# Kernel tuning notes

Measured on AMD Instinct MI355X. Metric: run time of the kernel, lower is better.

## Reference

```python
import jax, jax.numpy as jnp
import numpy as np

B, T, C = 2, 2048, 1024
NH = 16
HD = C // NH

def setup_inputs() -> dict:
    key = jax.random.key(0)
    k1, k2, k3 = jax.random.split(key, 3)
    x = jax.random.normal(k1, (B, T, C), dtype=jnp.float32)
    w_attn = jax.random.normal(k2, (C, 3 * C), dtype=jnp.float32) * 0.02
    w_proj = jax.random.normal(k3, (C, C), dtype=jnp.float32) * 0.02
    return {"x": x, "w_attn": w_attn, "w_proj": w_proj}

def reference(x, w_attn, w_proj):
    b, t, c = x.shape
    qkv = x @ w_attn                                  # [B,T,3C]
    q, k, v = jnp.split(qkv, 3, axis=-1)
    # [B,NH,T,HD]
    q = q.reshape(b, t, NH, HD).transpose(0, 2, 1, 3)
    k = k.reshape(b, t, NH, HD).transpose(0, 2, 1, 3)
    v = v.reshape(b, t, NH, HD).transpose(0, 2, 1, 3)
    scale = 1.0 / np.sqrt(HD).astype(np.float32)
    att = jnp.einsum('bhqd,bhkd->bhqk', q, k) * scale  # [B,NH,T,T]
    causal = jnp.tril(jnp.ones((t, t), dtype=bool))
    att = jnp.where(causal[None, None], att, jnp.float32(-jnp.inf))
    att = jax.nn.softmax(att, axis=-1)
    y = jnp.einsum('bhqk,bhkd->bhqd', att, v)          # [B,NH,T,HD]
    y = y.transpose(0, 2, 1, 3).reshape(b, t, c)
    return y @ w_proj
```

## Files before the change

kernel.cpp:

```cpp
#include <hip/hip_runtime.h>
#include <hip/hip_bf16.h>

#define BB 2
#define TT 2048
#define CCH 1024
#define NHH 16
#define HDD 64
#define M_TOK (BB*TT)
#define N_QKV (3*CCH)

typedef __attribute__((ext_vector_type(8))) short bf16x8;
typedef __attribute__((ext_vector_type(4))) float f32x4;
typedef unsigned short u16;
typedef unsigned int u32;

__device__ __forceinline__ u16 f2bf(float f) {
    union { float f; u32 u; } v; v.f = f;
    u32 u = v.u;
    u32 r = (u + 0x7FFFu + ((u >> 16) & 1u)) >> 16;
    return (u16)r;
}

__device__ __forceinline__ u32 pk_bf16(float a, float b) {
    u32 ua = __float_as_uint(a) + 0x8000u;
    u32 ub = __float_as_uint(b) + 0x8000u;
    return __builtin_amdgcn_perm(ub, ua, 0x07060302u);
}

__device__ __forceinline__ void async_copy16(const void* g, void* l) {
    __builtin_amdgcn_global_load_lds((__attribute__((address_space(1))) void*)g,
                                     (__attribute__((address_space(3))) void*)l,
                                     16, 0, 0);
}


__global__ __launch_bounds__(256) void cast_bf16_kernel(
    const float* __restrict__ src, u16* __restrict__ dst, int n4) {
    int i = blockIdx.x * 256 + threadIdx.x;
    if (i < n4) {
        float4 f = ((const float4*)src)[i];
        ushort4 o;
        o.x = f2bf(f.x); o.y = f2bf(f.y); o.z = f2bf(f.z); o.w = f2bf(f.w);
        ((ushort4*)dst)[i] = o;
    }
}

__global__ __launch_bounds__(256) void transpose_bf16_kernel(
    const float* __restrict__ src, u16* __restrict__ dst, int R, int Cn,
    int scale_rows, float sc) {
    __shared__ float tile[32][33];
    int c0 = blockIdx.x * 32, r0 = blockIdx.y * 32;
    int tx = threadIdx.x, ty = threadIdx.y;
#pragma unroll
    for (int i = ty; i < 32; i += 8)
        tile[i][tx] = src[(size_t)(r0 + i) * Cn + c0 + tx];
    __syncthreads();
#pragma unroll
    for (int i = ty; i < 32; i += 8) {
        float v = tile[tx][i];
        if (c0 + i < scale_rows) v *= sc;
        dst[(size_t)(c0 + i) * R + r0 + tx] = f2bf(v);
    }
}


template<int SWAP, int NJ>
__device__ __forceinline__ void gemm_kloop64(
    const u16* __restrict__ A, const u16* __restrict__ Bt, int K,
    int m0, int n0, int t, u16* __restrict__ As, u16* __restrict__ Bs,
    f32x4 (&acc)[4][4])
{
    int lane = t & 63, w = t >> 6;
    int mw = (w >> 1) * 64, nw = (w & 1) * (NJ * 16);
    int mr = lane & 15, quad = lane >> 4;
    int lr = lane >> 3;
    int cswz = (lane & 7) ^ lr;

    const u16* gA[4]; u16* lA[4];
#pragma unroll
    for (int p = 0; p < 4; ++p) {
        int grp = w * 4 + p;
        gA[p] = A + (size_t)(m0 + grp * 8 + lr) * K + cswz * 8;
        lA[p] = As + ((size_t)grp * 64 + lane) * 8;
    }
    const u16* gB[4]; u16* lB[4];
#pragma unroll
    for (int p = 0; p < NJ; ++p) {
        int grp = w * NJ + p;
        gB[p] = Bt + (size_t)(n0 + grp * 8 + lr) * K + cswz * 8;
        lB[p] = Bs + ((size_t)grp * 64 + lane) * 8;
    }

    int swm = mr & 7;
    for (int k0 = 0; k0 < K; k0 += 64) {
#pragma unroll
        for (int p = 0; p < 4; ++p) async_copy16(gA[p] + k0, lA[p]);
#pragma unroll
        for (int p = 0; p < NJ; ++p) async_copy16(gB[p] + k0, lB[p]);
        __syncthreads();
#pragma unroll
        for (int kk = 0; kk < 2; ++kk) {
            bf16x8 af[4], bfr[4];
#pragma unroll
            for (int i = 0; i < 4; ++i) {
                int r = mw + i * 16 + mr;
                af[i] = *(const bf16x8*)&As[r * 64 + (((kk * 4 + quad) ^ swm) << 3)];
            }
#pragma unroll
            for (int j = 0; j < NJ; ++j) {
                int r = nw + j * 16 + mr;
                bfr[j] = *(const bf16x8*)&Bs[r * 64 + (((kk * 4 + quad) ^ swm) << 3)];
            }
#pragma unroll
            for (int i = 0; i < 4; ++i)
#pragma unroll
                for (int j = 0; j < NJ; ++j) {
                    if (SWAP)
                        acc[i][j] = __builtin_amdgcn_mfma_f32_16x16x32_bf16(bfr[j], af[i], acc[i][j], 0, 0, 0);
                    else
                        acc[i][j] = __builtin_amdgcn_mfma_f32_16x16x32_bf16(af[i], bfr[j], acc[i][j], 0, 0, 0);
                }
        }
        __syncthreads();
    }
}


__global__ __launch_bounds__(256, 3) void qkv_gemm_kernel(
    const u16* __restrict__ A, const u16* __restrict__ Bt,
    u16* __restrict__ Qo, u16* __restrict__ Ko, u16* __restrict__ Vto)
{
    __shared__ u16 As[128 * 64];
    __shared__ u16 Bs[128 * 64];
    int t = threadIdx.x;
    int m0 = blockIdx.y * 128, n0 = blockIdx.x * 128;
    int part = n0 >> 10;
    int lane = t & 63, w = t >> 6;
    int mw = (w >> 1) * 64, nw = (w & 1) * 64;
    int mr = lane & 15, quad = lane >> 4;

    f32x4 zero = {0.f, 0.f, 0.f, 0.f};
    f32x4 acc[4][4];
#pragma unroll
    for (int i = 0; i < 4; ++i)
#pragma unroll
        for (int j = 0; j < 4; ++j) acc[i][j] = zero;

    if (part < 2) {
        gemm_kloop64<1, 4>(A, Bt, CCH, m0, n0, t, As, Bs, acc);
        u16* dstp = part ? Ko : Qo;
#pragma unroll
        for (int i = 0; i < 4; ++i)
#pragma unroll
            for (int j = 0; j < 4; ++j) {
                int tok = m0 + mw + i * 16 + mr;
                int cg0 = n0 + nw + j * 16 + quad * 4;
                int cc = cg0 & 1023;
                int h = cc >> 6, d0 = cc & 63;
                int b = tok >> 11, tt = tok & 2047;
                int bh = b * NHH + h;
                uint2 o;
                o.x = pk_bf16(acc[i][j][0], acc[i][j][1]);
                o.y = pk_bf16(acc[i][j][2], acc[i][j][3]);
                *(uint2*)&dstp[((size_t)bh * TT + tt) * HDD + d0] = o;
            }
    } else {
        gemm_kloop64<0, 4>(A, Bt, CCH, m0, n0, t, As, Bs, acc);
#pragma unroll
        for (int i = 0; i < 4; ++i)
#pragma unroll
            for (int j = 0; j < 4; ++j) {
                int t0 = m0 + mw + i * 16 + quad * 4;
                int cg = n0 + nw + j * 16 + mr;
                int cc = cg & 1023;
                int h = cc >> 6, d = cc & 63;
                int b = t0 >> 11, tt0 = t0 & 2047;
                int bh = b * NHH + h;
                uint2 o;
                o.x = pk_bf16(acc[i][j][0], acc[i][j][1]);
                o.y = pk_bf16(acc[i][j][2], acc[i][j][3]);
                *(uint2*)&Vto[((size_t)bh * HDD + d) * TT + tt0] = o;
            }
    }
}


__global__ __launch_bounds__(256) void proj_gemm_kernel(
    const u16* __restrict__ A, const u16* __restrict__ Bt, float* __restrict__ Cout)
{
    __shared__ u16 As[128 * 64];
    __shared__ u16 Bs[64 * 64];
    int t = threadIdx.x;
    int m0 = blockIdx.y * 128, n0 = blockIdx.x * 64;
    int lane = t & 63, w = t >> 6;
    int mw = (w >> 1) * 64, nw = (w & 1) * 32;
    int mr = lane & 15, quad = lane >> 4;

    f32x4 zero = {0.f, 0.f, 0.f, 0.f};
    f32x4 acc[4][4];
#pragma unroll
    for (int i = 0; i < 4; ++i)
#pragma unroll
        for (int j = 0; j < 4; ++j) acc[i][j] = zero;

    gemm_kloop64<1, 2>(A, Bt, CCH, m0, n0, t, As, Bs, acc);

#pragma unroll
    for (int i = 0; i < 4; ++i)
#pragma unroll
        for (int j = 0; j < 2; ++j) {
            int tok = m0 + mw + i * 16 + mr;
            int cg0 = n0 + nw + j * 16 + quad * 4;
            float4 v;
            v.x = acc[i][j][0]; v.y = acc[i][j][1];
            v.z = acc[i][j][2]; v.w = acc[i][j][3];
            *(float4*)&Cout[(size_t)tok * CCH + cg0] = v;
        }
}


#define PSTRIDE 72

template<bool MASK>
__device__ __forceinline__ void tile_compute(
    const bf16x8 (&kf)[4][2], const bf16x8 (&vf)[4][2], u16* __restrict__ pb,
    bf16x8 qf0, bf16x8 qf1, int m, int quad, int qcol, int kv0,
    f32x4 (&o)[4], f32x4& ls)
{
    f32x4 zero = {0.f, 0.f, 0.f, 0.f};
    f32x4 st[4];
#pragma unroll
    for (int kc = 0; kc < 4; ++kc) {
        f32x4 s = __builtin_amdgcn_mfma_f32_16x16x32_bf16(kf[kc][0], qf0, zero, 0, 0, 0);
        st[kc]   = __builtin_amdgcn_mfma_f32_16x16x32_bf16(kf[kc][1], qf1, s, 0, 0, 0);
    }
#pragma unroll
    for (int kc = 0; kc < 4; ++kc) {
        float e0, e1, e2, e3;
#pragma unroll
        for (int r = 0; r < 4; ++r) {
            float v = st[kc][r];
            if (MASK && (kv0 + kc * 16 + quad * 4 + r > qcol)) v = -1e30f;
            float e = __builtin_amdgcn_exp2f(v);
            ls[r] += e;
            if (r == 0) e0 = e; else if (r == 1) e1 = e; else if (r == 2) e2 = e; else e3 = e;
        }
        uint2 pk; pk.x = pk_bf16(e0, e1); pk.y = pk_bf16(e2, e3);
        *(uint2*)&pb[m * PSTRIDE + kc * 16 + quad * 4] = pk;
    }
#pragma unroll
    for (int ks = 0; ks < 2; ++ks) {
        bf16x8 pf = *(const bf16x8*)&pb[m * PSTRIDE + ks * 32 + quad * 8];
#pragma unroll
        for (int dg = 0; dg < 4; ++dg)
            o[dg] = __builtin_amdgcn_mfma_f32_16x16x32_bf16(vf[dg][ks], pf, o[dg], 0, 0, 0);
    }
}

__global__ __launch_bounds__(256) void attn_kernel(
    const u16* __restrict__ Q, const u16* __restrict__ K,
    const u16* __restrict__ Vt, u16* __restrict__ Y)
{
    __shared__ u16 Ks[64 * 64];
    __shared__ u16 Vs[64 * 64];
    __shared__ u16 Pl[4][16 * PSTRIDE];
    int t = threadIdx.x;
    int w = t >> 6, lane = t & 63;
    int m = lane & 15, quad = lane >> 4;

    int bid = blockIdx.x;
    int head = bid & 31;
    int g = bid >> 5;
    int pr = (g < 8) ? g : 23 - g;
    int qbA = pr;
    int qbB = 31 - pr;
    int rowA = qbA * 64 + w * 16;
    int rowB = qbB * 64 + w * 16;

    const u16* qpA = Q + ((size_t)head * TT + rowA + m) * HDD + quad * 8;
    const u16* qpB = Q + ((size_t)head * TT + rowB + m) * HDD + quad * 8;
    bf16x8 qA0 = *(const bf16x8*)qpA;
    bf16x8 qA1 = *(const bf16x8*)(qpA + 32);
    bf16x8 qB0 = *(const bf16x8*)qpB;
    bf16x8 qB1 = *(const bf16x8*)(qpB + 32);

    const u16* kbase = K + (size_t)head * TT * HDD;
    const u16* vbase = Vt + (size_t)head * HDD * TT;
    u16* pb = &Pl[w][0];

    int lr = lane >> 3;
    int cg = (lane & 7) ^ lr;
    int r0 = w * 16 + lr, r1 = r0 + 8;
    u16* ldsK0 = Ks + (size_t)(w * 128 + lane) * 8;
    u16* ldsK1 = Ks + (size_t)(w * 128 + 64 + lane) * 8;
    u16* ldsV0 = Vs + (size_t)(w * 128 + lane) * 8;
    u16* ldsV1 = Vs + (size_t)(w * 128 + 64 + lane) * 8;

    f32x4 zero = {0.f, 0.f, 0.f, 0.f};
    f32x4 oA[4], oB[4], lsA = zero, lsB = zero;
#pragma unroll
    for (int dg = 0; dg < 4; ++dg) { oA[dg] = zero; oB[dg] = zero; }
    int qcolA = rowA + m, qcolB = rowB + m;
    int sw = m & 7;

    for (int ic = 0; ic <= qbB; ++ic) {
        int kv0 = ic << 6;
        async_copy16(kbase + (size_t)(kv0 + r0) * 64 + cg * 8, ldsK0);
        async_copy16(kbase + (size_t)(kv0 + r1) * 64 + cg * 8, ldsK1);
        async_copy16(vbase + (size_t)r0 * TT + kv0 + cg * 8, ldsV0);
        async_copy16(vbase + (size_t)r1 * TT + kv0 + cg * 8, ldsV1);
        __syncthreads();
        bf16x8 kf[4][2], vf[4][2];
#pragma unroll
        for (int kc = 0; kc < 4; ++kc) {
            int rr = kc * 16 + m;
            kf[kc][0] = *(const bf16x8*)&Ks[rr * 64 + ((quad ^ sw) << 3)];
            kf[kc][1] = *(const bf16x8*)&Ks[rr * 64 + (((quad + 4) ^ sw) << 3)];
            vf[kc][0] = *(const bf16x8*)&Vs[rr * 64 + ((quad ^ sw) << 3)];
            vf[kc][1] = *(const bf16x8*)&Vs[rr * 64 + (((quad + 4) ^ sw) << 3)];
        }
        if (ic < qbA)
            tile_compute<false>(kf, vf, pb, qA0, qA1, m, quad, qcolA, kv0, oA, lsA);
        else if (ic == qbA)
            tile_compute<true>(kf, vf, pb, qA0, qA1, m, quad, qcolA, kv0, oA, lsA);
        if (ic < qbB)
            tile_compute<false>(kf, vf, pb, qB0, qB1, m, quad, qcolB, kv0, oB, lsB);
        else
            tile_compute<true>(kf, vf, pb, qB0, qB1, m, quad, qcolB, kv0, oB, lsB);
        __syncthreads();
    }

    float lA = (lsA[0] + lsA[1]) + (lsA[2] + lsA[3]);
    float lB = (lsB[0] + lsB[1]) + (lsB[2] + lsB[3]);
    lA += __shfl_xor(lA, 16, 64); lA += __shfl_xor(lA, 32, 64);
    lB += __shfl_xor(lB, 16, 64); lB += __shfl_xor(lB, 32, 64);
    float invA = 1.0f / lA, invB = 1.0f / lB;

    int b = head >> 4, h = head & 15;
    size_t roA = ((size_t)(b * TT + rowA + m)) * CCH + h * HDD;
    size_t roB = ((size_t)(b * TT + rowB + m)) * CCH + h * HDD;
#pragma unroll
    for (int dg = 0; dg < 4; ++dg) {
        uint2 ov;
        ov.x = pk_bf16(oA[dg][0] * invA, oA[dg][1] * invA);
        ov.y = pk_bf16(oA[dg][2] * invA, oA[dg][3] * invA);
        *(uint2*)&Y[roA + dg * 16 + quad * 4] = ov;
        ov.x = pk_bf16(oB[dg][0] * invB, oB[dg][1] * invB);
        ov.y = pk_bf16(oB[dg][2] * invB, oB[dg][3] * invB);
        *(uint2*)&Y[roB + dg * 16 + quad * 4] = ov;
    }
}


extern "C" void kernel_launch(void* const* d_in, const int* in_sizes, int n_in,
                              void* d_out, int out_size, void* d_ws, size_t ws_size,
                              hipStream_t stream) {
    const float* x      = (const float*)d_in[0];
    const float* w_attn = (const float*)d_in[1];
    const float* w_proj = (const float*)d_in[2];
    float* out = (float*)d_out;

    char* ws = (char*)d_ws;
    u16* x_bf   = (u16*)ws; ws += (size_t)M_TOK * CCH * 2;
    u16* wqkvT  = (u16*)ws; ws += (size_t)N_QKV * CCH * 2;
    u16* wprojT = (u16*)ws; ws += (size_t)CCH * CCH * 2;
    u16* qbuf   = (u16*)ws; ws += (size_t)BB * NHH * TT * HDD * 2;
    u16* kbuf   = (u16*)ws; ws += (size_t)BB * NHH * TT * HDD * 2;
    u16* vtb    = (u16*)ws; ws += (size_t)BB * NHH * HDD * TT * 2;
    u16* yb     = (u16*)ws; ws += (size_t)M_TOK * CCH * 2;

    const float QSC = 0.125f * 1.44269504088896f;

    cast_bf16_kernel<<<dim3(M_TOK * CCH / 4 / 256), dim3(256), 0, stream>>>(x, x_bf, M_TOK * CCH / 4);
    transpose_bf16_kernel<<<dim3(N_QKV / 32, CCH / 32), dim3(32, 8), 0, stream>>>(
        w_attn, wqkvT, CCH, N_QKV, CCH, QSC);
    transpose_bf16_kernel<<<dim3(CCH / 32, CCH / 32), dim3(32, 8), 0, stream>>>(
        w_proj, wprojT, CCH, CCH, 0, 1.0f);
    qkv_gemm_kernel<<<dim3(24, 32), dim3(256), 0, stream>>>(
        x_bf, wqkvT, qbuf, kbuf, vtb);
    attn_kernel<<<dim3(512), dim3(256), 0, stream>>>(qbuf, kbuf, vtb, yb);
    proj_gemm_kernel<<<dim3(16, 32), dim3(256), 0, stream>>>(yb, wprojT, out);
}
```

Baseline: 173.8 us.

## Double-buffer K/V tiles in LDS to prefetch the next tile during compute

The attention kernel now keeps two LDS buffers each for K and V. It issues the async global-to-LDS copies for the next KV tile right after the per-iteration barrier, so the loads overlap with the current tile's MFMA and softmax work. The trailing barrier is removed, leaving one sync per iteration. The cost is twice the K/V LDS footprint, which may lower occupancy, and the barrier at the top of each iteration now has to wait for the prefetched copies.

Result: no change. 174.3 us (+0.3%).

```diff
diff --git a/kernel.cpp b/kernel.cpp
--- a/kernel.cpp
+++ b/kernel.cpp
@@ -261,8 +261,8 @@
     const u16* __restrict__ Q, const u16* __restrict__ K,
     const u16* __restrict__ Vt, u16* __restrict__ Y)
 {
-    __shared__ u16 Ks[64 * 64];
-    __shared__ u16 Vs[64 * 64];
+    __shared__ u16 Ks[2][64 * 64];
+    __shared__ u16 Vs[2][64 * 64];
     __shared__ u16 Pl[4][16 * PSTRIDE];
     int t = threadIdx.x;
     int w = t >> 6, lane = t & 63;
@@ -291,10 +291,8 @@
     int lr = lane >> 3;
     int cg = (lane & 7) ^ lr;
     int r0 = w * 16 + lr, r1 = r0 + 8;
-    u16* ldsK0 = Ks + (size_t)(w * 128 + lane) * 8;
-    u16* ldsK1 = Ks + (size_t)(w * 128 + 64 + lane) * 8;
-    u16* ldsV0 = Vs + (size_t)(w * 128 + lane) * 8;
-    u16* ldsV1 = Vs + (size_t)(w * 128 + 64 + lane) * 8;
+    int loff0 = (w * 128 + lane) * 8;
+    int loff1 = (w * 128 + 64 + lane) * 8;
 
     f32x4 zero = {0.f, 0.f, 0.f, 0.f};
     f32x4 oA[4], oB[4], lsA = zero, lsB = zero;
@@ -303,21 +301,32 @@
     int qcolA = rowA + m, qcolB = rowB + m;
     int sw = m & 7;
 
+    async_copy16(kbase + (size_t)r0 * 64 + cg * 8, &Ks[0][loff0]);
+    async_copy16(kbase + (size_t)r1 * 64 + cg * 8, &Ks[0][loff1]);
+    async_copy16(vbase + (size_t)r0 * TT + cg * 8, &Vs[0][loff0]);
+    async_copy16(vbase + (size_t)r1 * TT + cg * 8, &Vs[0][loff1]);
+
     for (int ic = 0; ic <= qbB; ++ic) {
+        int buf = ic & 1;
         int kv0 = ic << 6;
-        async_copy16(kbase + (size_t)(kv0 + r0) * 64 + cg * 8, ldsK0);
-        async_copy16(kbase + (size_t)(kv0 + r1) * 64 + cg * 8, ldsK1);
-        async_copy16(vbase + (size_t)r0 * TT + kv0 + cg * 8, ldsV0);
-        async_copy16(vbase + (size_t)r1 * TT + kv0 + cg * 8, ldsV1);
         __syncthreads();
+        if (ic < qbB) {
+            int nkv = kv0 + 64;
+            async_copy16(kbase + (size_t)(nkv + r0) * 64 + cg * 8, &Ks[buf ^ 1][loff0]);
+            async_copy16(kbase + (size_t)(nkv + r1) * 64 + cg * 8, &Ks[buf ^ 1][loff1]);
+            async_copy16(vbase + (size_t)r0 * TT + nkv + cg * 8, &Vs[buf ^ 1][loff0]);
+            async_copy16(vbase + (size_t)r1 * TT + nkv + cg * 8, &Vs[buf ^ 1][loff1]);
+        }
+        const u16* Kb = Ks[buf];
+        const u16* Vb = Vs[buf];
         bf16x8 kf[4][2], vf[4][2];
 #pragma unroll
         for (int kc = 0; kc < 4; ++kc) {
             int rr = kc * 16 + m;
-            kf[kc][0] = *(const bf16x8*)&Ks[rr * 64 + ((quad ^ sw) << 3)];
-            kf[kc][1] = *(const bf16x8*)&Ks[rr * 64 + (((quad + 4) ^ sw) << 3)];
-            vf[kc][0] = *(const bf16x8*)&Vs[rr * 64 + ((quad ^ sw) << 3)];
-            vf[kc][1] = *(const bf16x8*)&Vs[rr * 64 + (((quad + 4) ^ sw) << 3)];
+            kf[kc][0] = *(const bf16x8*)&Kb[rr * 64 + ((quad ^ sw) << 3)];
+            kf[kc][1] = *(const bf16x8*)&Kb[rr * 64 + (((quad + 4) ^ sw) << 3)];
+            vf[kc][0] = *(const bf16x8*)&Vb[rr * 64 + ((quad ^ sw) << 3)];
+            vf[kc][1] = *(const bf16x8*)&Vb[rr * 64 + (((quad + 4) ^ sw) << 3)];
         }
         if (ic < qbA)
             tile_compute<false>(kf, vf, pb, qA0, qA1, m, quad, qcolA, kv0, oA, lsA);
@@ -327,7 +336,6 @@
             tile_compute<false>(kf, vf, pb, qB0, qB1, m, quad, qcolB, kv0, oB, lsB);
         else
             tile_compute<true>(kf, vf, pb, qB0, qB1, m, quad, qcolB, kv0, oB, lsB);
-        __syncthreads();
     }
 
     float lA = (lsA[0] + lsA[1]) + (lsA[2] + lsA[3]);
```
